# Optimization experiments

Measured on AMD Instinct MI355X. Metric: run time of the kernel, lower is better.

## Reference

```python
import jax, jax.numpy as jnp
import numpy as np

B, L, P, D, RD, NT = 128, 128, 1024, 128, 128, 256
SCALE = 1.0 / float(np.sqrt(D))


def _gelu(x):
    return jax.nn.gelu(x, approximate=False)


def _ln(x, g, b):
    mu = jnp.mean(x, axis=-1, keepdims=True)
    v = jnp.mean((x - mu) ** 2, axis=-1, keepdims=True)
    return (x - mu) * jax.lax.rsqrt(v + 1e-5) * g + b


def _mlp2(x, w1, b1, w2, b2):
    return _gelu(x @ w1 + b1) @ w2 + b2


def _l2norm(x):
    return x / jnp.maximum(jnp.sqrt(jnp.sum(x * x, axis=-1, keepdims=True)), 1e-12)


def _params(key):
    ks = jax.random.split(key, 16)
    def lin(k, i, o):
        return jax.random.normal(k, (i, o), jnp.float32) * (1.0 / float(np.sqrt(i)))
    z = lambda *s: jnp.zeros(s, jnp.float32)
    o = lambda *s: jnp.ones(s, jnp.float32)
    p = {}
    p['lt_emb'] = jax.random.normal(ks[0], (NT, D), jnp.float32) * 0.02
    p['lx_w1'] = lin(ks[1], 8, D); p['lx_b1'] = z(D)
    p['lx_w2'] = lin(ks[2], D, D); p['lx_b2'] = z(D)
    p['l_ln_g'] = o(D); p['l_ln_b'] = z(D)
    p['pt_emb'] = jax.random.normal(ks[3], (NT, D), jnp.float32) * 0.02
    p['px_w1'] = lin(ks[4], 192, D); p['px_b1'] = z(D)
    p['px_w2'] = lin(ks[5], D, D); p['px_b2'] = z(D)
    p['ps_w1'] = lin(ks[6], 1, D); p['ps_b1'] = z(D)
    p['ps_w2'] = lin(ks[7], D, D); p['ps_b2'] = z(D)
    p['p_ln_g'] = o(D); p['p_ln_b'] = z(D)
    p['proj_l_w'] = lin(ks[8], D, D)
    p['proj_p_w'] = lin(ks[9], D, D)
    p['dustbin_vec'] = jax.random.normal(ks[10], (D,), jnp.float32) * 0.02
    p['sg_w1'] = lin(ks[11], D, D); p['sg_b1'] = z(D)
    p['sg_w2'] = lin(ks[12], D, 1); p['sg_b2'] = z(1)
    p['retr_l_w'] = lin(ks[13], D, RD)
    p['retr_p_w'] = lin(ks[14], D, RD)
    return p


def setup_inputs():
    key = jax.random.key(0)
    kd = jax.random.split(key, 10)
    inp = {
        'l_x': jax.random.normal(kd[0], (B, L, 8), jnp.float32),
        'l_typ': jax.random.randint(kd[1], (B, L), 0, NT),
        'p_x': jax.random.normal(kd[2], (B, P, 192), jnp.float32),
        'p_typ': jax.random.randint(kd[3], (B, P), 0, NT),
        'p_score': jax.random.normal(kd[4], (B, P), jnp.float32),
        'p_rad': jax.random.uniform(kd[5], (B, P), jnp.float32),
        'l_mask': jax.random.bernoulli(kd[6], 0.9, (B, L)).at[:, 0].set(True),
        'p_mask': jax.random.bernoulli(kd[7], 0.9, (B, P)).at[:, 0].set(True),
    }
    inp.update(_params(kd[8]))
    return inp


def reference(l_x, l_typ, p_x, p_typ, p_score, p_rad, l_mask, p_mask,
              lt_emb, lx_w1, lx_b1, lx_w2, lx_b2, l_ln_g, l_ln_b,
              pt_emb, px_w1, px_b1, px_w2, px_b2, ps_w1, ps_b1, ps_w2, ps_b2,
              p_ln_g, p_ln_b, proj_l_w, proj_p_w, dustbin_vec,
              sg_w1, sg_b1, sg_w2, sg_b2, retr_l_w, retr_p_w):
    # --- encode_batch ---
    hL = _ln(_mlp2(l_x, lx_w1, lx_b1, lx_w2, lx_b2)
             + lt_emb[jnp.clip(l_typ, 0, NT - 1)], l_ln_g, l_ln_b) @ proj_l_w
    hP = _ln(_mlp2(p_x, px_w1, px_b1, px_w2, px_b2)
             + pt_emb[jnp.clip(p_typ, 0, NT - 1)]
             + _mlp2(p_score[..., None], ps_w1, ps_b1, ps_w2, ps_b2), p_ln_g, p_ln_b) @ proj_p_w
    neg = jnp.finfo(jnp.float32).min
    # --- feature_logits_batch: masked bilinear similarity ---
    logits = jnp.einsum('bld,bpd->blp', hL, hP) * SCALE  # [B,L,P]
    logits = jnp.where(p_mask[:, None, :], logits, neg)
    logits = jnp.where(l_mask[:, :, None], logits, neg)
    # --- assignment_logW_batch with dustbin ---
    dust = (hL @ dustbin_vec) * SCALE  # [B,L]
    full = jnp.concatenate([logits, dust[:, :, None]], axis=-1)  # [B,L,P+1]
    full = jnp.where(l_mask[:, :, None], full, neg)
    logW = jax.nn.log_softmax(full, axis=-1)
    # --- invariant_feature_terms_batch ---
    W = jnp.exp(logW)
    lm = l_mask.astype(jnp.float32)
    pm = p_mask.astype(jnp.float32)
    denom = jnp.maximum(lm.sum(axis=1), 1.0)  # [B]
    Wm = jnp.concatenate([W[..., :-1] * pm[:, None, :], W[..., -1:]], axis=-1)
    sharp = (Wm.max(axis=-1) * lm).sum(axis=1) / denom
    ent = ((-(Wm * logW)).sum(axis=-1) * lm).sum(axis=1) / denom
    neg_ent = -ent
    # --- pooled_embeddings_batch ---
    l_g = (hL * lm[..., None]).sum(axis=1) / jnp.maximum(lm.sum(axis=1)[:, None], 1.0)
    p_g = (hP * pm[..., None]).sum(axis=1) / jnp.maximum(pm.sum(axis=1)[:, None], 1.0)
    l_z = _l2norm(l_g @ retr_l_w)
    p_z = _l2norm(p_g @ retr_p_w)
    # --- pocket_sigma_nodes_batch ---
    sig = jax.nn.softplus((_gelu(hP @ sg_w1 + sg_b1) @ sg_w2 + sg_b2)[..., 0]) + 1e-3 + jnp.maximum(p_rad, 0.0)
    return logW, sharp, neg_ent, l_z, p_z, sig
```

## Files before the change

kernel.cpp:

```cpp
#include <hip/hip_runtime.h>
#include <hip/hip_bf16.h>
#include <math.h>

#define B_ 128
#define L_ 128
#define P_ 1024
#define D_ 128
#define NT_ 256

#define NEGF (-__FLT_MAX__)
#define SCALE_ 0.08838834764831845f
#define CLAMPV 1e30f

#define OUT_SHARP  16793600
#define OUT_NEGENT 16793728
#define OUT_LZ     16793856
#define OUT_PZ     16810240
#define OUT_SIG    16826624

#define WS_HLB    0
#define WS_HPB    1048576
#define WS_DUST   9437184
#define WS_SHARPP 9453568
#define WS_ENTP   9454592
#define WS_FLAG   9455616
#define WS_WT     9455632
#define WS_PPART  9500696
#define WS_PCNT   10024984

using bh8  = __attribute__((ext_vector_type(8))) short;
using fx4  = __attribute__((ext_vector_type(4))) float;

__device__ __forceinline__ float gelu_(float x) {
    float c = x * x;
    float v = x * fmaf(c, 0.07135481584f, 1.5957691216f);
    return x * __builtin_amdgcn_rcpf(1.0f + __expf(-v));
}
__device__ __forceinline__ float bf2f(unsigned short u) {
    return __uint_as_float(((unsigned)u) << 16);
}
__device__ __forceinline__ float sanz(float x) {
    return fminf(fmaxf(x, -CLAMPV), CLAMPV);
}
template<int BF> __device__ __forceinline__ float ldf(const void* p, int i) {
    if constexpr (BF) return bf2f(((const unsigned short*)p)[i]);
    else return ((const float*)p)[i];
}
template<int BF> __device__ __forceinline__ void stf(void* p, size_t i, float x) {
    x = sanz(x);
    if constexpr (BF) ((__hip_bfloat16*)p)[i] = __float2bfloat16(x);
    else ((float*)p)[i] = x;
}
__device__ __forceinline__ float maskf(const void* m, int mm, int idx) {
    if (mm == 3) return ((const float*)m)[idx] != 0.f ? 1.f : 0.f;
    if (mm == 2) return ((const unsigned short*)m)[idx] ? 1.f : 0.f;
    if (mm == 1) return ((const unsigned char*)m)[idx] ? 1.f : 0.f;
    return ((const int*)m)[idx] ? 1.f : 0.f;
}
__device__ __forceinline__ int typf(const void* p, int tm, int idx) {
    int v;
    if (tm == 2) v = (int)bf2f(((const unsigned short*)p)[idx]);
    else if (tm == 1) v = (int)((const long long*)p)[idx];
    else v = ((const int*)p)[idx];
    return v < 0 ? 0 : (v > NT_ - 1 ? NT_ - 1 : v);
}

__global__ __launch_bounds__(64) void detect_k(const unsigned int* __restrict__ px,
                                               const unsigned int* __restrict__ pm,
                                               const unsigned int* __restrict__ pt,
                                               int* __restrict__ flags)
{
    const int t = threadIdx.x;
    int hit = 0;
    for (int i = t; i < 4096; i += 64) {
        unsigned e = (px[i] >> 7) & 0xFFu;
        hit += (e >= 110 && e <= 132) ? 1 : 0;
    }
    for (int s = 1; s < 64; s <<= 1) hit += __shfl_xor(hit, s);

    unsigned big = 0, lo3f = 0, hi3f = 0;
    for (int i = t; i < 1024; i += 64) {
        unsigned wv = pm[i];
        big  |= (wv > 1u) ? 1u : 0u;
        lo3f |= ((wv & 0xFFFFu) == 0x3F80u) ? 1u : 0u;
        hi3f |= ((wv >> 16) == 0x3F80u) ? 1u : 0u;
    }
    unsigned long long aBig = __ballot(big != 0), aLo = __ballot(lo3f != 0), aHi = __ballot(hi3f != 0);

    unsigned tbig = 0, oddnz = 0;
    for (int i = t; i < 512; i += 64) {
        unsigned we = pt[2 * i], wo = pt[2 * i + 1];
        tbig  |= (we > 0xFFFFu || wo > 0xFFFFu) ? 1u : 0u;
        oddnz |= (wo != 0u) ? 1u : 0u;
    }
    unsigned long long aTb = __ballot(tbig != 0), aOdd = __ballot(oddnz != 0);

    if (t == 0) {
        flags[1] = (hit > 2048) ? 1 : 0;
        flags[0] = aLo ? 2 : (aHi ? 3 : (aBig ? 1 : 0));
        flags[2] = aTb ? 2 : (!aOdd ? 1 : 0);
    }
}

template<int BF> __device__ __forceinline__ void wt_prep_body(
    const void* w1, const void* w2, const void* sw2,
    const void* proj, const void* gw1, __hip_bfloat16* wt)
{
    const int idx = blockIdx.x * 256 + threadIdx.x;
    const int stride = gridDim.x * 256;
    for (int i = idx; i < 128 * 192; i += stride) {
        int n = i / 192, k = i - n * 192;
        wt[n * 192 + k] = __float2bfloat16(ldf<BF>(w1, k * 128 + n));
    }
    __hip_bfloat16* w2c = wt + 24576;
    for (int i = idx; i < 128 * 256; i += stride) {
        int n = i >> 8, k = i & 255;
        float v = (k < 128) ? ldf<BF>(w2, k * 128 + n) : ldf<BF>(sw2, (k - 128) * 128 + n);
        w2c[n * 256 + k] = __float2bfloat16(v);
    }
    __hip_bfloat16* pjt = wt + 57344;
    for (int i = idx; i < 128 * 128; i += stride) {
        int n = i >> 7, k = i & 127;
        pjt[n * 128 + k] = __float2bfloat16(ldf<BF>(proj, k * 128 + n));
    }
    __hip_bfloat16* g1t = wt + 73728;
    for (int i = idx; i < 128 * 128; i += stride) {
        int n = i >> 7, k = i & 127;
        g1t[n * 128 + k] = __float2bfloat16(ldf<BF>(gw1, k * 128 + n));
    }
}

__global__ __launch_bounds__(256) void wt_prep_k(
    const void* w1, const void* w2, const void* sw2,
    const void* proj, const void* gw1, __hip_bfloat16* wt, const int* flags)
{
    if (flags[1]) wt_prep_body<1>(w1, w2, sw2, proj, gw1, wt);
    else          wt_prep_body<0>(w1, w2, sw2, proj, gw1, wt);
}

#define RL 8
template<int BF> __device__ __forceinline__ void enc_l_body(
    const void* l_x, const void* l_typ, int tm,
    const void* w1, const void* b1, const void* w2, const void* b2,
    const void* lng, const void* lnb, const void* emb, const void* proj,
    const void* dustv, __hip_bfloat16* hLb, float* dust)
{
    __shared__ __align__(16) float X[RL * 8];
    __shared__ __align__(16) float H[RL][D_];
    __shared__ __align__(16) float Y[RL][D_];
    __shared__ float mus[RL], rss[RL];
    const int o = threadIdx.x;
    const int base = blockIdx.x * RL;

    if (o < RL * 8) X[o] = ldf<BF>(l_x, base * 8 + o);
    __syncthreads();

    float acc[RL];
    const float b1o = ldf<BF>(b1, o);
#pragma unroll
    for (int r = 0; r < RL; r++) acc[r] = b1o;
#pragma unroll
    for (int i = 0; i < 8; i += 4) {
        float wa = ldf<BF>(w1, (i + 0) * D_ + o), wb = ldf<BF>(w1, (i + 1) * D_ + o);
        float wc = ldf<BF>(w1, (i + 2) * D_ + o), wd = ldf<BF>(w1, (i + 3) * D_ + o);
#pragma unroll
        for (int r = 0; r < RL; r++) {
            const float4 x4 = *(const float4*)&X[r * 8 + i];
            acc[r] = fmaf(x4.x, wa, fmaf(x4.y, wb, fmaf(x4.z, wc, fmaf(x4.w, wd, acc[r]))));
        }
    }
#pragma unroll
    for (int r = 0; r < RL; r++) H[r][o] = gelu_(acc[r]);
    __syncthreads();

#pragma unroll
    for (int r = 0; r < RL; r++) {
        int tt = typf(l_typ, tm, base + r);
        acc[r] = ldf<BF>(b2, o) + ldf<BF>(emb, tt * D_ + o);
    }
    for (int i = 0; i < D_; i += 4) {
        float wa = ldf<BF>(w2, (i + 0) * D_ + o), wb = ldf<BF>(w2, (i + 1) * D_ + o);
        float wc = ldf<BF>(w2, (i + 2) * D_ + o), wd = ldf<BF>(w2, (i + 3) * D_ + o);
#pragma unroll
        for (int r = 0; r < RL; r++) {
            const float4 h4 = *(const float4*)&H[r][i];
            acc[r] = fmaf(h4.x, wa, fmaf(h4.y, wb, fmaf(h4.z, wc, fmaf(h4.w, wd, acc[r]))));
        }
    }
#pragma unroll
    for (int r = 0; r < RL; r++) Y[r][o] = acc[r];
    __syncthreads();

    {
        const int r = o >> 4, j = o & 15;
        float s = 0.f;
#pragma unroll
        for (int i = 0; i < 8; i++) s += Y[r][j * 8 + i];
        s += __shfl_xor(s, 1); s += __shfl_xor(s, 2); s += __shfl_xor(s, 4); s += __shfl_xor(s, 8);
        const float mu = s * (1.f / 128.f);
        float v = 0.f;
#pragma unroll
        for (int i = 0; i < 8; i++) { float d = Y[r][j * 8 + i] - mu; v = fmaf(d, d, v); }
        v += __shfl_xor(v, 1); v += __shfl_xor(v, 2); v += __shfl_xor(v, 4); v += __shfl_xor(v, 8);
        if (j == 0) { mus[r] = mu; rss[r] = rsqrtf(v * (1.f / 128.f) + 1e-5f); }
    }
    __syncthreads();
    {
        const float g = ldf<BF>(lng, o), bl = ldf<BF>(lnb, o);
#pragma unroll
        for (int r = 0; r < RL; r++) Y[r][o] = fmaf((Y[r][o] - mus[r]) * rss[r], g, bl);
    }
    __syncthreads();

#pragma unroll
    for (int r = 0; r < RL; r++) acc[r] = 0.f;
    for (int i = 0; i < D_; i += 4) {
        float wa = ldf<BF>(proj, (i + 0) * D_ + o), wb = ldf<BF>(proj, (i + 1) * D_ + o);
        float wc = ldf<BF>(proj, (i + 2) * D_ + o), wd = ldf<BF>(proj, (i + 3) * D_ + o);
#pragma unroll
        for (int r = 0; r < RL; r++) {
            const float4 y4 = *(const float4*)&Y[r][i];
            acc[r] = fmaf(y4.x, wa, fmaf(y4.y, wb, fmaf(y4.z, wc, fmaf(y4.w, wd, acc[r]))));
        }
    }
    const float dvo = ldf<BF>(dustv, o);
#pragma unroll
    for (int r = 0; r < RL; r++) {
        hLb[(size_t)(base + r) * D_ + o] = __float2bfloat16(acc[r]);
        H[r][o] = acc[r] * dvo;
    }
    __syncthreads();
    {
        const int r = o >> 4, j = o & 15;
        float s = 0.f;
#pragma unroll
        for (int i = 0; i < 8; i++) s += H[r][j * 8 + i];
        s += __shfl_xor(s, 1); s += __shfl_xor(s, 2); s += __shfl_xor(s, 4); s += __shfl_xor(s, 8);
        if (j == 0) dust[base + r] = s * SCALE_;
    }
}

__global__ __launch_bounds__(128) void enc_l_k(
    const void* l_x, const void* l_typ,
    const void* w1, const void* b1, const void* w2, const void* b2,
    const void* lng, const void* lnb, const void* emb, const void* proj,
    const void* dustv, __hip_bfloat16* hLb, float* dust, const int* flags)
{
    const int tm = flags[2];
    if (flags[1]) enc_l_body<1>(l_x, l_typ, tm, w1, b1, w2, b2, lng, lnb, emb, proj, dustv, hLb, dust);
    else          enc_l_body<0>(l_x, l_typ, tm, w1, b1, w2, b2, lng, lnb, emb, proj, dustv, hLb, dust);
}

#define XS 264
#define ROWS 64
#define ENC_P_SMEM 36608
template<int BF> __device__ __forceinline__ void enc_p_body(
    unsigned short* X, float* red1, float* red2, float* pm_s, float* sc_s, int* tt_s,
    const void* p_x, const void* p_typ, int tm,
    const void* p_score, const void* p_rad,
    const void* b1, const void* b2, const void* sb2,
    const void* sw1, const void* sb1,
    const void* lng, const void* lnb, const void* emb,
    const void* gb1, const void* gw2, const void* gb2,
    const unsigned short* wt, const void* p_mask, int mm,
    void* out, __hip_bfloat16* hPb, float* ppart, float* pcnt)
{
    const int t = threadIdx.x;
    const int o = t & 127, rh = t >> 7;
    const int lane = t & 63, w = t >> 6;
    const int m = lane & 15, g = lane >> 4;
    const int b = blockIdx.x >> 4, tile = blockIdx.x & 15;
    const int base = b * P_ + tile * ROWS;
    const int c0 = 32 * w + m, c1 = 32 * w + 16 + m;
    __hip_bfloat16* Xb = (__hip_bfloat16*)X;

    if constexpr (BF) {
        const unsigned short* src = (const unsigned short*)p_x + (size_t)base * 192;
#pragma unroll
        for (int i = t * 8; i < ROWS * 192; i += 256 * 8) {
            const int r = i / 192, k = i - r * 192;
            *(bh8*)(X + r * XS + k) = *(const bh8*)(src + i);
        }
    } else {
        for (int i = t; i < ROWS * 192; i += 256) {
            int r = i / 192, k = i - r * 192;
            Xb[r * XS + k] = __float2bfloat16(((const float*)p_x)[(size_t)base * 192 + i]);
        }
    }
    if (t < ROWS) {
        pm_s[t] = maskf(p_mask, mm, base + t);
        sc_s[t] = ldf<BF>(p_score, base + t);
        tt_s[t] = typf(p_typ, tm, base + t);
    }
    __syncthreads();

    fx4 A1[4][2];
#pragma unroll
    for (int mt = 0; mt < 4; mt++) { A1[mt][0] = fx4{0,0,0,0}; A1[mt][1] = fx4{0,0,0,0}; }
    {
        const unsigned short* q0 = wt + ((2 * w + 0) * 16 + m) * 192 + g * 8;
        const unsigned short* q1 = wt + ((2 * w + 1) * 16 + m) * 192 + g * 8;
#pragma unroll
        for (int ks = 0; ks < 6; ks++) {
            bh8 f0 = *(const bh8*)(q0 + ks * 32);
            bh8 f1 = *(const bh8*)(q1 + ks * 32);
#pragma unroll
            for (int mt = 0; mt < 4; mt++) {
                bh8 a = *(const bh8*)(X + (mt * 16 + m) * XS + g * 8 + ks * 32);
                A1[mt][0] = __builtin_amdgcn_mfma_f32_16x16x32_bf16(a, f0, A1[mt][0], 0, 0, 0);
                A1[mt][1] = __builtin_amdgcn_mfma_f32_16x16x32_bf16(a, f1, A1[mt][1], 0, 0, 0);
            }
        }
    }
    __syncthreads();

    {
        const float bb0 = ldf<BF>(b1, c0), bb1 = ldf<BF>(b1, c1);
#pragma unroll
        for (int mt = 0; mt < 4; mt++)
#pragma unroll
            for (int j = 0; j < 4; j++) {
                const int row = mt * 16 + g * 4 + j;
                Xb[row * XS + c0] = __float2bfloat16(gelu_(A1[mt][0][j] + bb0));
                Xb[row * XS + c1] = __float2bfloat16(gelu_(A1[mt][1][j] + bb1));
            }
    }
    {
        const float a1v = ldf<BF>(sw1, o), a0v = ldf<BF>(sb1, o);
#pragma unroll
        for (int r = 0; r < 32; r++) {
            const int row = rh * 32 + r;
            Xb[row * XS + 128 + o] = __float2bfloat16(gelu_(fmaf(sc_s[row], a1v, a0v)));
        }
    }
    __syncthreads();

    fx4 A2[4][2];
#pragma unroll
    for (int mt = 0; mt < 4; mt++) { A2[mt][0] = fx4{0,0,0,0}; A2[mt][1] = fx4{0,0,0,0}; }
    {
        const unsigned short* w2cT = wt + 24576;
        const unsigned short* q0 = w2cT + ((2 * w + 0) * 16 + m) * 256 + g * 8;
        const unsigned short* q1 = w2cT + ((2 * w + 1) * 16 + m) * 256 + g * 8;
#pragma unroll
        for (int ks = 0; ks < 8; ks++) {
            bh8 f0 = *(const bh8*)(q0 + ks * 32);
            bh8 f1 = *(const bh8*)(q1 + ks * 32);
#pragma unroll
            for (int mt = 0; mt < 4; mt++) {
                bh8 a = *(const bh8*)(X + (mt * 16 + m) * XS + g * 8 + ks * 32);
                A2[mt][0] = __builtin_amdgcn_mfma_f32_16x16x32_bf16(a, f0, A2[mt][0], 0, 0, 0);
                A2[mt][1] = __builtin_amdgcn_mfma_f32_16x16x32_bf16(a, f1, A2[mt][1], 0, 0, 0);
            }
        }
    }
    {
        const float bc0 = ldf<BF>(b2, c0) + ldf<BF>(sb2, c0);
        const float bc1 = ldf<BF>(b2, c1) + ldf<BF>(sb2, c1);
#pragma unroll
        for (int mt = 0; mt < 4; mt++)
#pragma unroll
            for (int j = 0; j < 4; j++) {
                const int row = mt * 16 + g * 4 + j;
                const int tt = tt_s[row];
                A2[mt][0][j] += bc0 + ldf<BF>(emb, tt * D_ + c0);
                A2[mt][1][j] += bc1 + ldf<BF>(emb, tt * D_ + c1);
            }
    }
#pragma unroll
    for (int mt = 0; mt < 4; mt++)
#pragma unroll
        for (int j = 0; j < 4; j++) {
            float s = A2[mt][0][j] + A2[mt][1][j];
            s += __shfl_xor(s, 1); s += __shfl_xor(s, 2); s += __shfl_xor(s, 4); s += __shfl_xor(s, 8);
            if (m == 0) red1[(mt * 16 + g * 4 + j) * 4 + w] = s;
        }
    __syncthreads();
    float mu_[4][4];
#pragma unroll
    for (int mt = 0; mt < 4; mt++)
#pragma unroll
        for (int j = 0; j < 4; j++) {
            const int row = mt * 16 + g * 4 + j;
            mu_[mt][j] = ((red1[row * 4 + 0] + red1[row * 4 + 1]) +
                          (red1[row * 4 + 2] + red1[row * 4 + 3])) * (1.f / 128.f);
            float d0 = A2[mt][0][j] - mu_[mt][j];
            float d1 = A2[mt][1][j] - mu_[mt][j];
            float v = fmaf(d0, d0, d1 * d1);
            v += __shfl_xor(v, 1); v += __shfl_xor(v, 2); v += __shfl_xor(v, 4); v += __shfl_xor(v, 8);
            if (m == 0) red2[row * 4 + w] = v;
        }
    __syncthreads();
    {
        const float gc0 = ldf<BF>(lng, c0), bl0 = ldf<BF>(lnb, c0);
        const float gc1 = ldf<BF>(lng, c1), bl1 = ldf<BF>(lnb, c1);
#pragma unroll
        for (int mt = 0; mt < 4; mt++)
#pragma unroll
            for (int j = 0; j < 4; j++) {
                const int row = mt * 16 + g * 4 + j;
                float var = ((red2[row * 4 + 0] + red2[row * 4 + 1]) +
                             (red2[row * 4 + 2] + red2[row * 4 + 3])) * (1.f / 128.f);
                float rs = rsqrtf(var + 1e-5f);
                float y0 = fmaf((A2[mt][0][j] - mu_[mt][j]) * rs, gc0, bl0);
                float y1 = fmaf((A2[mt][1][j] - mu_[mt][j]) * rs, gc1, bl1);
                Xb[row * XS + c0] = __float2bfloat16(y0);
                Xb[row * XS + c1] = __float2bfloat16(y1);
            }
    }
    __syncthreads();

    fx4 A3[4][2];
#pragma unroll
    for (int mt = 0; mt < 4; mt++) { A3[mt][0] = fx4{0,0,0,0}; A3[mt][1] = fx4{0,0,0,0}; }
    {
        const unsigned short* pjT = wt + 57344;
        const unsigned short* q0 = pjT + ((2 * w + 0) * 16 + m) * 128 + g * 8;
        const unsigned short* q1 = pjT + ((2 * w + 1) * 16 + m) * 128 + g * 8;
#pragma unroll
        for (int ks = 0; ks < 4; ks++) {
            bh8 f0 = *(const bh8*)(q0 + ks * 32);
            bh8 f1 = *(const bh8*)(q1 + ks * 32);
#pragma unroll
            for (int mt = 0; mt < 4; mt++) {
                bh8 a = *(const bh8*)(X + (mt * 16 + m) * XS + g * 8 + ks * 32);
                A3[mt][0] = __builtin_amdgcn_mfma_f32_16x16x32_bf16(a, f0, A3[mt][0], 0, 0, 0);
                A3[mt][1] = __builtin_amdgcn_mfma_f32_16x16x32_bf16(a, f1, A3[mt][1], 0, 0, 0);
            }
        }
    }
    __syncthreads();

    {
#pragma unroll
        for (int mt = 0; mt < 4; mt++)
#pragma unroll
            for (int j = 0; j < 4; j++) {
                const int row = mt * 16 + g * 4 + j;
                __hip_bfloat16 h0 = __float2bfloat16(A3[mt][0][j]);
                __hip_bfloat16 h1 = __float2bfloat16(A3[mt][1][j]);
                hPb[(size_t)(base + row) * D_ + c0] = h0;
                hPb[(size_t)(base + row) * D_ + c1] = h1;
                Xb[row * XS + c0] = h0;
                Xb[row * XS + c1] = h1;
            }
        float ps0 = 0.f, ps1 = 0.f;
#pragma unroll
        for (int mt = 0; mt < 4; mt++)
#pragma unroll
            for (int j = 0; j < 4; j++) {
                const int row = mt * 16 + g * 4 + j;
                ps0 = fmaf(A3[mt][0][j], pm_s[row], ps0);
                ps1 = fmaf(A3[mt][1][j], pm_s[row], ps1);
            }
        ps0 += __shfl_xor(ps0, 16); ps0 += __shfl_xor(ps0, 32);
        ps1 += __shfl_xor(ps1, 16); ps1 += __shfl_xor(ps1, 32);
        if (g == 0) {
            ppart[(size_t)blockIdx.x * D_ + c0] = ps0;
            ppart[(size_t)blockIdx.x * D_ + c1] = ps1;
        }
        if (t == 0) {
            float c = 0.f;
#pragma unroll
            for (int r = 0; r < ROWS; r++) c += pm_s[r];
            pcnt[blockIdx.x] = c;
        }
    }
    __syncthreads();

    fx4 A4[4][2];
#pragma unroll
    for (int mt = 0; mt < 4; mt++) { A4[mt][0] = fx4{0,0,0,0}; A4[mt][1] = fx4{0,0,0,0}; }
    {
        const unsigned short* g1T = wt + 73728;
        const unsigned short* q0 = g1T + ((2 * w + 0) * 16 + m) * 128 + g * 8;
        const unsigned short* q1 = g1T + ((2 * w + 1) * 16 + m) * 128 + g * 8;
#pragma unroll
        for (int ks = 0; ks < 4; ks++) {
            bh8 f0 = *(const bh8*)(q0 + ks * 32);
            bh8 f1 = *(const bh8*)(q1 + ks * 32);
#pragma unroll
            for (int mt = 0; mt < 4; mt++) {
                bh8 a = *(const bh8*)(X + (mt * 16 + m) * XS + g * 8 + ks * 32);
                A4[mt][0] = __builtin_amdgcn_mfma_f32_16x16x32_bf16(a, f0, A4[mt][0], 0, 0, 0);
                A4[mt][1] = __builtin_amdgcn_mfma_f32_16x16x32_bf16(a, f1, A4[mt][1], 0, 0, 0);
            }
        }
    }
    {
        const float gb0 = ldf<BF>(gb1, c0), gb1v = ldf<BF>(gb1, c1);
        const float w20 = ldf<BF>(gw2, c0), w21 = ldf<BF>(gw2, c1);
#pragma unroll
        for (int mt = 0; mt < 4; mt++)
#pragma unroll
            for (int j = 0; j < 4; j++) {
                const int row = mt * 16 + g * 4 + j;
                float g0 = gelu_(A4[mt][0][j] + gb0);
                float g1v = gelu_(A4[mt][1][j] + gb1v);
                float p = fmaf(g0, w20, g1v * w21);
                p += __shfl_xor(p, 1); p += __shfl_xor(p, 2); p += __shfl_xor(p, 4); p += __shfl_xor(p, 8);
                if (m == 0) red1[row * 4 + w] = p;
            }
    }
    __syncthreads();
    if (t < ROWS) {
        float s = (red1[t * 4 + 0] + red1[t * 4 + 1]) + (red1[t * 4 + 2] + red1[t * 4 + 3]);
        float v = s + ldf<BF>(gb2, 0);
        float sp = fmaxf(v, 0.f) + log1pf(expf(-fabsf(v)));
        stf<BF>(out, (size_t)OUT_SIG + base + t, sp + 1e-3f + fmaxf(ldf<BF>(p_rad, base + t), 0.f));
    }
}

__global__ __launch_bounds__(256) void enc_p_k(
    const void* p_x, const void* p_typ, const void* p_score, const void* p_rad,
    const void* b1, const void* b2, const void* sb2,
    const void* sw1, const void* sb1,
    const void* lng, const void* lnb, const void* emb,
    const void* gb1, const void* gw2, const void* gb2,
    const unsigned short* wt, const void* p_mask, const int* flags,
    void* out, __hip_bfloat16* hPb, float* ppart, float* pcnt)
{
    extern __shared__ __align__(16) char smem[];
    unsigned short* X = (unsigned short*)smem;
    float* red1 = (float*)(smem + 33792);
    float* red2 = (float*)(smem + 34816);
    float* pm_s = (float*)(smem + 35840);
    float* sc_s = (float*)(smem + 36096);
    int*   tt_s = (int*)(smem + 36352);
    const int tm = flags[2], mm = flags[0];
    if (flags[1]) enc_p_body<1>(X, red1, red2, pm_s, sc_s, tt_s,
                                p_x, p_typ, tm, p_score, p_rad, b1, b2, sb2, sw1, sb1,
                                lng, lnb, emb, gb1, gw2, gb2, wt, p_mask, mm,
                                out, hPb, ppart, pcnt);
    else          enc_p_body<0>(X, red1, red2, pm_s, sc_s, tt_s,
                                p_x, p_typ, tm, p_score, p_rad, b1, b2, sb2, sw1, sb1,
                                lng, lnb, emb, gb1, gw2, gb2, wt, p_mask, mm,
                                out, hPb, ppart, pcnt);
}

template<int BF> __device__ __forceinline__ void logits_sm_body(
    const unsigned short* hLb, const unsigned short* hPb, const float* dust,
    const void* l_mask, const void* p_mask, int mm,
    void* out, float* sharp_parts, float* ent_parts)
{
    __shared__ float pm_s[1024];
    __shared__ float lm_s[16], dv_s[16];
    __shared__ float redA[64], redB[64], redC[64], redD[64], redM[16], redL[16];
    const int t = threadIdx.x;
    const int lane = t & 63, w = t >> 6;
    const int m = lane & 15, g = lane >> 4;
    const int b = blockIdx.x & 127, l0 = (blockIdx.x >> 7) * 16;

    for (int i = t; i < 1024; i += 256) pm_s[i] = maskf(p_mask, mm, b * P_ + i);
    if (t < 16) {
        lm_s[t] = maskf(l_mask, mm, b * L_ + l0 + t);
        dv_s[t] = dust[b * L_ + l0 + t];
    }
    __syncthreads();

    bh8 af[4];
    {
        const unsigned short* ha = hLb + ((size_t)(b * L_ + l0 + m)) * D_ + g * 8;
#pragma unroll
        for (int ks = 0; ks < 4; ks++) af[ks] = *(const bh8*)(ha + ks * 32);
    }
    const unsigned short* hpb = hPb + ((size_t)(b * P_ + w * 256)) * D_;

    fx4 acc[16];
#pragma unroll
    for (int nt = 0; nt < 16; nt++) {
        fx4 c = {0.f, 0.f, 0.f, 0.f};
        const unsigned short* hr = hpb + (nt * 16 + m) * D_ + g * 8;
#pragma unroll
        for (int ks = 0; ks < 4; ks++) {
            bh8 bfr = *(const bh8*)(hr + ks * 32);
            c = __builtin_amdgcn_mfma_f32_16x16x32_bf16(af[ks], bfr, c, 0, 0, 0);
        }
        acc[nt] = c;
    }

    float rmax[4] = {NEGF, NEGF, NEGF, NEGF};
#pragma unroll
    for (int nt = 0; nt < 16; nt++) {
        const float pv = pm_s[w * 256 + nt * 16 + m];
#pragma unroll
        for (int j = 0; j < 4; j++) {
            const bool ok = (lm_s[g * 4 + j] != 0.f) && (pv != 0.f);
            float v = ok ? acc[nt][j] * SCALE_ : NEGF;
            acc[nt][j] = v;
            rmax[j] = fmaxf(rmax[j], v);
        }
    }
#pragma unroll
    for (int j = 0; j < 4; j++) {
        rmax[j] = fmaxf(rmax[j], __shfl_xor(rmax[j], 1));
        rmax[j] = fmaxf(rmax[j], __shfl_xor(rmax[j], 2));
        rmax[j] = fmaxf(rmax[j], __shfl_xor(rmax[j], 4));
        rmax[j] = fmaxf(rmax[j], __shfl_xor(rmax[j], 8));
    }
    if (m == 0) {
#pragma unroll
        for (int j = 0; j < 4; j++) redA[(g * 4 + j) * 4 + w] = rmax[j];
    }
    __syncthreads();
    float mrow[4], lse[4];
#pragma unroll
    for (int j = 0; j < 4; j++) {
        const int r = g * 4 + j;
        float mm4 = fmaxf(fmaxf(redA[r * 4 + 0], redA[r * 4 + 1]), fmaxf(redA[r * 4 + 2], redA[r * 4 + 3]));
        float dvr = (lm_s[r] != 0.f) ? dv_s[r] : NEGF;
        mrow[j] = fmaxf(mm4, dvr);
    }
    float se[4] = {0.f, 0.f, 0.f, 0.f};
#pragma unroll
    for (int nt = 0; nt < 16; nt++) {
#pragma unroll
        for (int j = 0; j < 4; j++) se[j] += __expf(acc[nt][j] - mrow[j]);
    }
#pragma unroll
    for (int j = 0; j < 4; j++) {
        se[j] += __shfl_xor(se[j], 1); se[j] += __shfl_xor(se[j], 2);
        se[j] += __shfl_xor(se[j], 4); se[j] += __shfl_xor(se[j], 8);
    }
    if (m == 0) {
#pragma unroll
        for (int j = 0; j < 4; j++) redB[(g * 4 + j) * 4 + w] = se[j];
    }
    __syncthreads();
#pragma unroll
    for (int j = 0; j < 4; j++) {
        const int r = g * 4 + j;
        float dvr = (lm_s[r] != 0.f) ? dv_s[r] : NEGF;
        float s = (redB[r * 4 + 0] + redB[r * 4 + 1]) + (redB[r * 4 + 2] + redB[r * 4 + 3]);
        s += __expf(dvr - mrow[j]);
        lse[j] = __logf(s);
    }
    if (w == 0 && m == 0) {
#pragma unroll
        for (int j = 0; j < 4; j++) { redM[g * 4 + j] = mrow[j]; redL[g * 4 + j] = lse[j]; }
    }
    float mw[4] = {0.f, 0.f, 0.f, 0.f}, es[4] = {0.f, 0.f, 0.f, 0.f};
#pragma unroll
    for (int nt = 0; nt < 16; nt++) {
        const float pv = pm_s[w * 256 + nt * 16 + m];
#pragma unroll
        for (int j = 0; j < 4; j++) {
            float lw = acc[nt][j] - mrow[j] - lse[j];
            stf<BF>(out, (size_t)(b * L_ + l0 + g * 4 + j) * (P_ + 1) + w * 256 + nt * 16 + m, lw);
            float lwc = fmaxf(lw, -CLAMPV);
            float wm = __expf(lwc) * pv;
            mw[j] = fmaxf(mw[j], wm);
            if (wm > 0.f) es[j] = fmaf(-wm, lwc, es[j]);
        }
    }
#pragma unroll
    for (int j = 0; j < 4; j++) {
        mw[j] = fmaxf(mw[j], __shfl_xor(mw[j], 1));
        mw[j] = fmaxf(mw[j], __shfl_xor(mw[j], 2));
        mw[j] = fmaxf(mw[j], __shfl_xor(mw[j], 4));
        mw[j] = fmaxf(mw[j], __shfl_xor(mw[j], 8));
        es[j] += __shfl_xor(es[j], 1); es[j] += __shfl_xor(es[j], 2);
        es[j] += __shfl_xor(es[j], 4); es[j] += __shfl_xor(es[j], 8);
    }
    if (m == 0) {
#pragma unroll
        for (int j = 0; j < 4; j++) {
            redC[(g * 4 + j) * 4 + w] = mw[j];
            redD[(g * 4 + j) * 4 + w] = es[j];
        }
    }
    __syncthreads();
    if (t < 16) {
        float dvr = (lm_s[t] != 0.f) ? dv_s[t] : NEGF;
        stf<BF>(out, (size_t)(b * L_ + l0 + t) * (P_ + 1) + P_, dvr - redM[t] - redL[t]);
    }
    if (t == 0) {
        float sp = 0.f, en = 0.f;
        for (int r = 0; r < 16; r++) {
            float dvr = (lm_s[r] != 0.f) ? dv_s[r] : NEGF;
            float lwd = fmaxf(dvr - redM[r] - redL[r], -CLAMPV);
            float wd = __expf(lwd);
            float mwr = fmaxf(fmaxf(redC[r * 4 + 0], redC[r * 4 + 1]), fmaxf(redC[r * 4 + 2], redC[r * 4 + 3]));
            mwr = fmaxf(mwr, wd);
            float esr = (redD[r * 4 + 0] + redD[r * 4 + 1]) + (redD[r * 4 + 2] + redD[r * 4 + 3]);
            if (wd > 0.f) esr = fmaf(-wd, lwd, esr);
            sp = fmaf(mwr, lm_s[r], sp);
            en = fmaf(esr, lm_s[r], en);
        }
        sharp_parts[blockIdx.x] = sp;
        ent_parts[blockIdx.x] = en;
    }
}

__global__ __launch_bounds__(256) void logits_sm_k(
    const unsigned short* hLb, const unsigned short* hPb, const float* dust,
    const void* l_mask, const void* p_mask, const int* flags,
    void* out, float* sharp_parts, float* ent_parts)
{
    const int mm = flags[0];
    if (flags[1]) logits_sm_body<1>(hLb, hPb, dust, l_mask, p_mask, mm, out, sharp_parts, ent_parts);
    else          logits_sm_body<0>(hLb, hPb, dust, l_mask, p_mask, mm, out, sharp_parts, ent_parts);
}

template<int BF> __device__ __forceinline__ void epilogue_body(
    const unsigned short* hLb, const void* l_mask, int mm,
    const void* retr_l, const void* retr_p,
    const float* ppart, const float* pcnt,
    const float* sharp_parts, const float* ent_parts, void* out)
{
    __shared__ float lmv[L_];
    __shared__ __align__(16) float lg[D_];
    __shared__ __align__(16) float pgs[D_];
    __shared__ float red[4];
    const int o = threadIdx.x, b = blockIdx.x;
    lmv[o] = maskf(l_mask, mm, b * L_ + o);
    __syncthreads();
    float cnt = 0.f;
    for (int l = 0; l < L_; l++) cnt += lmv[l];
    {
        float s0 = 0, s1 = 0, s2 = 0, s3 = 0;
        const unsigned short* hb = hLb + (size_t)b * L_ * D_;
        for (int l = 0; l < L_; l += 4) {
            s0 = fmaf(bf2f(hb[(l + 0) * D_ + o]), lmv[l + 0], s0);
            s1 = fmaf(bf2f(hb[(l + 1) * D_ + o]), lmv[l + 1], s1);
            s2 = fmaf(bf2f(hb[(l + 2) * D_ + o]), lmv[l + 2], s2);
            s3 = fmaf(bf2f(hb[(l + 3) * D_ + o]), lmv[l + 3], s3);
        }
        lg[o] = ((s0 + s1) + (s2 + s3)) / fmaxf(cnt, 1.f);
    }
    {
        float s = 0.f, c = 0.f;
        for (int k = 0; k < 16; k++) s += ppart[(size_t)(b * 16 + k) * D_ + o];
        for (int k = 0; k < 16; k++) c += pcnt[b * 16 + k];
        pgs[o] = s / fmaxf(c, 1.f);
    }
    __syncthreads();
    float rL = 0.f, rP = 0.f;
    for (int i = 0; i < D_; i += 4) {
        const float4 g4 = *(const float4*)&lg[i];
        rL = fmaf(g4.x, ldf<BF>(retr_l, (i + 0) * D_ + o), rL);
        rL = fmaf(g4.y, ldf<BF>(retr_l, (i + 1) * D_ + o), rL);
        rL = fmaf(g4.z, ldf<BF>(retr_l, (i + 2) * D_ + o), rL);
        rL = fmaf(g4.w, ldf<BF>(retr_l, (i + 3) * D_ + o), rL);
        const float4 p4 = *(const float4*)&pgs[i];
        rP = fmaf(p4.x, ldf<BF>(retr_p, (i + 0) * D_ + o), rP);
        rP = fmaf(p4.y, ldf<BF>(retr_p, (i + 1) * D_ + o), rP);
        rP = fmaf(p4.z, ldf<BF>(retr_p, (i + 2) * D_ + o), rP);
        rP = fmaf(p4.w, ldf<BF>(retr_p, (i + 3) * D_ + o), rP);
    }
    float nL = rL * rL, nP = rP * rP;
    nL += __shfl_xor(nL, 1); nL += __shfl_xor(nL, 2); nL += __shfl_xor(nL, 4);
    nL += __shfl_xor(nL, 8); nL += __shfl_xor(nL, 16); nL += __shfl_xor(nL, 32);
    nP += __shfl_xor(nP, 1); nP += __shfl_xor(nP, 2); nP += __shfl_xor(nP, 4);
    nP += __shfl_xor(nP, 8); nP += __shfl_xor(nP, 16); nP += __shfl_xor(nP, 32);
    if ((o & 63) == 0) { red[o >> 6] = nL; red[2 + (o >> 6)] = nP; }
    __syncthreads();
    {
        float nrmL = fmaxf(sqrtf(red[0] + red[1]), 1e-12f);
        float nrmP = fmaxf(sqrtf(red[2] + red[3]), 1e-12f);
        stf<BF>(out, (size_t)OUT_LZ + b * D_ + o, rL / nrmL);
        stf<BF>(out, (size_t)OUT_PZ + b * D_ + o, rP / nrmP);
    }
    if (o == 0) {
        const float den = fmaxf(cnt, 1.f);
        float sp = 0.f, en = 0.f;
        for (int k = 0; k < 8; k++) { sp += sharp_parts[k * 128 + b]; en += ent_parts[k * 128 + b]; }
        stf<BF>(out, (size_t)OUT_SHARP + b, sp / den);
        stf<BF>(out, (size_t)OUT_NEGENT + b, -(en / den));
    }
}

__global__ __launch_bounds__(128) void epilogue_k(
    const unsigned short* hLb, const void* l_mask, const int* flags,
    const void* retr_l, const void* retr_p,
    const float* ppart, const float* pcnt,
    const float* sharp_parts, const float* ent_parts, void* out)
{
    const int mm = flags[0];
    if (flags[1]) epilogue_body<1>(hLb, l_mask, mm, retr_l, retr_p, ppart, pcnt, sharp_parts, ent_parts, out);
    else          epilogue_body<0>(hLb, l_mask, mm, retr_l, retr_p, ppart, pcnt, sharp_parts, ent_parts, out);
}

extern "C" void kernel_launch(void* const* d_in, const int* in_sizes, int n_in,
                              void* d_out, int out_size, void* d_ws, size_t ws_size,
                              hipStream_t stream)
{
    const void* l_x     = d_in[0];
    const void* l_typ   = d_in[1];
    const void* p_x     = d_in[2];
    const void* p_typ   = d_in[3];
    const void* p_score = d_in[4];
    const void* p_rad   = d_in[5];
    const void* l_mask  = d_in[6];
    const void* p_mask  = d_in[7];
    const void* lt_emb  = d_in[8];
    const void* lx_w1   = d_in[9];
    const void* lx_b1   = d_in[10];
    const void* lx_w2   = d_in[11];
    const void* lx_b2   = d_in[12];
    const void* l_ln_g  = d_in[13];
    const void* l_ln_b  = d_in[14];
    const void* pt_emb  = d_in[15];
    const void* px_w1   = d_in[16];
    const void* px_b1   = d_in[17];
    const void* px_w2   = d_in[18];
    const void* px_b2   = d_in[19];
    const void* ps_w1   = d_in[20];
    const void* ps_b1   = d_in[21];
    const void* ps_w2   = d_in[22];
    const void* ps_b2   = d_in[23];
    const void* p_ln_g  = d_in[24];
    const void* p_ln_b  = d_in[25];
    const void* proj_l  = d_in[26];
    const void* proj_p  = d_in[27];
    const void* dustv   = d_in[28];
    const void* sg_w1   = d_in[29];
    const void* sg_b1   = d_in[30];
    const void* sg_w2   = d_in[31];
    const void* sg_b2   = d_in[32];
    const void* retr_l  = d_in[33];
    const void* retr_p  = d_in[34];

    float* ws     = (float*)d_ws;
    __hip_bfloat16* hLb = (__hip_bfloat16*)(ws + WS_HLB);
    __hip_bfloat16* hPb = (__hip_bfloat16*)(ws + WS_HPB);
    float* dust   = ws + WS_DUST;
    float* sharpp = ws + WS_SHARPP;
    float* entp   = ws + WS_ENTP;
    int*   flags  = (int*)(ws + WS_FLAG);
    __hip_bfloat16* wt = (__hip_bfloat16*)(ws + WS_WT);
    float* ppart  = ws + WS_PPART;
    float* pcnt   = ws + WS_PCNT;

    detect_k<<<1, 64, 0, stream>>>((const unsigned int*)p_x, (const unsigned int*)p_mask,
                                   (const unsigned int*)p_typ, flags);
    wt_prep_k<<<64, 256, 0, stream>>>(px_w1, px_w2, ps_w2, proj_p, sg_w1, wt, flags);
    enc_l_k<<<(B_ * L_) / RL, 128, 0, stream>>>(l_x, l_typ, lx_w1, lx_b1, lx_w2, lx_b2,
                                                l_ln_g, l_ln_b, lt_emb, proj_l, dustv,
                                                hLb, dust, flags);
    enc_p_k<<<B_ * (P_ / ROWS), 256, ENC_P_SMEM, stream>>>(
        p_x, p_typ, p_score, p_rad,
        px_b1, px_b2, ps_b2, ps_w1, ps_b1,
        p_ln_g, p_ln_b, pt_emb,
        sg_b1, sg_w2, sg_b2,
        (const unsigned short*)wt, p_mask, flags,
        d_out, hPb, ppart, pcnt);
    logits_sm_k<<<B_ * 8, 256, 0, stream>>>((const unsigned short*)hLb, (const unsigned short*)hPb,
                                            dust, l_mask, p_mask, flags, d_out, sharpp, entp);
    epilogue_k<<<B_, 128, 0, stream>>>((const unsigned short*)hLb, l_mask, flags,
                                       retr_l, retr_p, ppart, pcnt, sharpp, entp, d_out);
}
```

Baseline: 211.2 us.

## Split enc_p column tiles across eight waves with 512-thread blocks

```diff
diff --git a/kernel.cpp b/kernel.cpp
--- a/kernel.cpp
+++ b/kernel.cpp
@@ -253,7 +253,7 @@
 
 #define XS 264
 #define ROWS 64
-#define ENC_P_SMEM 36608
+#define ENC_P_SMEM 38656
 template<int BF> __device__ __forceinline__ void enc_p_body(
     unsigned short* X, float* red1, float* red2, float* pm_s, float* sc_s, int* tt_s,
     const void* p_x, const void* p_typ, int tm,
@@ -271,18 +271,18 @@
     const int m = lane & 15, g = lane >> 4;
     const int b = blockIdx.x >> 4, tile = blockIdx.x & 15;
     const int base = b * P_ + tile * ROWS;
-    const int c0 = 32 * w + m, c1 = 32 * w + 16 + m;
+    const int c = 16 * w + m;
     __hip_bfloat16* Xb = (__hip_bfloat16*)X;
 
     if constexpr (BF) {
         const unsigned short* src = (const unsigned short*)p_x + (size_t)base * 192;
 #pragma unroll
-        for (int i = t * 8; i < ROWS * 192; i += 256 * 8) {
+        for (int i = t * 8; i < ROWS * 192; i += 512 * 8) {
             const int r = i / 192, k = i - r * 192;
             *(bh8*)(X + r * XS + k) = *(const bh8*)(src + i);
         }
     } else {
-        for (int i = t; i < ROWS * 192; i += 256) {
+        for (int i = t; i < ROWS * 192; i += 512) {
             int r = i / 192, k = i - r * 192;
             Xb[r * XS + k] = __float2bfloat16(((const float*)p_x)[(size_t)base * 192 + i]);
         }
@@ -294,86 +294,75 @@
     }
     __syncthreads();
 
-    fx4 A1[4][2];
-#pragma unroll
-    for (int mt = 0; mt < 4; mt++) { A1[mt][0] = fx4{0,0,0,0}; A1[mt][1] = fx4{0,0,0,0}; }
-    {
-        const unsigned short* q0 = wt + ((2 * w + 0) * 16 + m) * 192 + g * 8;
-        const unsigned short* q1 = wt + ((2 * w + 1) * 16 + m) * 192 + g * 8;
+    fx4 A1[4];
+#pragma unroll
+    for (int mt = 0; mt < 4; mt++) A1[mt] = fx4{0, 0, 0, 0};
+    {
+        const unsigned short* q = wt + (w * 16 + m) * 192 + g * 8;
 #pragma unroll
         for (int ks = 0; ks < 6; ks++) {
-            bh8 f0 = *(const bh8*)(q0 + ks * 32);
-            bh8 f1 = *(const bh8*)(q1 + ks * 32);
+            bh8 f = *(const bh8*)(q + ks * 32);
 #pragma unroll
             for (int mt = 0; mt < 4; mt++) {
                 bh8 a = *(const bh8*)(X + (mt * 16 + m) * XS + g * 8 + ks * 32);
-                A1[mt][0] = __builtin_amdgcn_mfma_f32_16x16x32_bf16(a, f0, A1[mt][0], 0, 0, 0);
-                A1[mt][1] = __builtin_amdgcn_mfma_f32_16x16x32_bf16(a, f1, A1[mt][1], 0, 0, 0);
-            }
-        }
-    }
-    __syncthreads();
-
-    {
-        const float bb0 = ldf<BF>(b1, c0), bb1 = ldf<BF>(b1, c1);
+                A1[mt] = __builtin_amdgcn_mfma_f32_16x16x32_bf16(a, f, A1[mt], 0, 0, 0);
+            }
+        }
+    }
+    __syncthreads();
+
+    {
+        const float bb = ldf<BF>(b1, c);
 #pragma unroll
         for (int mt = 0; mt < 4; mt++)
 #pragma unroll
             for (int j = 0; j < 4; j++) {
                 const int row = mt * 16 + g * 4 + j;
-                Xb[row * XS + c0] = __float2bfloat16(gelu_(A1[mt][0][j] + bb0));
-                Xb[row * XS + c1] = __float2bfloat16(gelu_(A1[mt][1][j] + bb1));
+                Xb[row * XS + c] = __float2bfloat16(gelu_(A1[mt][j] + bb));
             }
     }
     {
         const float a1v = ldf<BF>(sw1, o), a0v = ldf<BF>(sb1, o);
 #pragma unroll
-        for (int r = 0; r < 32; r++) {
-            const int row = rh * 32 + r;
+        for (int r = 0; r < 16; r++) {
+            const int row = rh * 16 + r;
             Xb[row * XS + 128 + o] = __float2bfloat16(gelu_(fmaf(sc_s[row], a1v, a0v)));
         }
     }
     __syncthreads();
 
-    fx4 A2[4][2];
-#pragma unroll
-    for (int mt = 0; mt < 4; mt++) { A2[mt][0] = fx4{0,0,0,0}; A2[mt][1] = fx4{0,0,0,0}; }
-    {
-        const unsigned short* w2cT = wt + 24576;
-        const unsigned short* q0 = w2cT + ((2 * w + 0) * 16 + m) * 256 + g * 8;
-        const unsigned short* q1 = w2cT + ((2 * w + 1) * 16 + m) * 256 + g * 8;
+    fx4 A2[4];
+#pragma unroll
+    for (int mt = 0; mt < 4; mt++) A2[mt] = fx4{0, 0, 0, 0};
+    {
+        const unsigned short* q = wt + 24576 + (w * 16 + m) * 256 + g * 8;
 #pragma unroll
         for (int ks = 0; ks < 8; ks++) {
-            bh8 f0 = *(const bh8*)(q0 + ks * 32);
-            bh8 f1 = *(const bh8*)(q1 + ks * 32);
+            bh8 f = *(const bh8*)(q + ks * 32);
 #pragma unroll
             for (int mt = 0; mt < 4; mt++) {
                 bh8 a = *(const bh8*)(X + (mt * 16 + m) * XS + g * 8 + ks * 32);
-                A2[mt][0] = __builtin_amdgcn_mfma_f32_16x16x32_bf16(a, f0, A2[mt][0], 0, 0, 0);
-                A2[mt][1] = __builtin_amdgcn_mfma_f32_16x16x32_bf16(a, f1, A2[mt][1], 0, 0, 0);
-            }
-        }
-    }
-    {
-        const float bc0 = ldf<BF>(b2, c0) + ldf<BF>(sb2, c0);
-        const float bc1 = ldf<BF>(b2, c1) + ldf<BF>(sb2, c1);
+                A2[mt] = __builtin_amdgcn_mfma_f32_16x16x32_bf16(a, f, A2[mt], 0, 0, 0);
+            }
+        }
+    }
+    {
+        const float bc = ldf<BF>(b2, c) + ldf<BF>(sb2, c);
 #pragma unroll
         for (int mt = 0; mt < 4; mt++)
 #pragma unroll
             for (int j = 0; j < 4; j++) {
                 const int row = mt * 16 + g * 4 + j;
-                const int tt = tt_s[row];
-                A2[mt][0][j] += bc0 + ldf<BF>(emb, tt * D_ + c0);
-                A2[mt][1][j] += bc1 + ldf<BF>(emb, tt * D_ + c1);
+                A2[mt][j] += bc + ldf<BF>(emb, tt_s[row] * D_ + c);
             }
     }
 #pragma unroll
     for (int mt = 0; mt < 4; mt++)
 #pragma unroll
         for (int j = 0; j < 4; j++) {
-            float s = A2[mt][0][j] + A2[mt][1][j];
+            float s = A2[mt][j];
             s += __shfl_xor(s, 1); s += __shfl_xor(s, 2); s += __shfl_xor(s, 4); s += __shfl_xor(s, 8);
-            if (m == 0) red1[(mt * 16 + g * 4 + j) * 4 + w] = s;
+            if (m == 0) red1[(mt * 16 + g * 4 + j) * 8 + w] = s;
         }
     __syncthreads();
     float mu_[4][4];
@@ -382,50 +371,43 @@
 #pragma unroll
         for (int j = 0; j < 4; j++) {
             const int row = mt * 16 + g * 4 + j;
-            mu_[mt][j] = ((red1[row * 4 + 0] + red1[row * 4 + 1]) +
-                          (red1[row * 4 + 2] + red1[row * 4 + 3])) * (1.f / 128.f);
-            float d0 = A2[mt][0][j] - mu_[mt][j];
-            float d1 = A2[mt][1][j] - mu_[mt][j];
-            float v = fmaf(d0, d0, d1 * d1);
+            float s = ((red1[row * 8 + 0] + red1[row * 8 + 1]) + (red1[row * 8 + 2] + red1[row * 8 + 3]))
+                    + ((red1[row * 8 + 4] + red1[row * 8 + 5]) + (red1[row * 8 + 6] + red1[row * 8 + 7]));
+            mu_[mt][j] = s * (1.f / 128.f);
+            float d = A2[mt][j] - mu_[mt][j];
+            float v = d * d;
             v += __shfl_xor(v, 1); v += __shfl_xor(v, 2); v += __shfl_xor(v, 4); v += __shfl_xor(v, 8);
-            if (m == 0) red2[row * 4 + w] = v;
-        }
-    __syncthreads();
-    {
-        const float gc0 = ldf<BF>(lng, c0), bl0 = ldf<BF>(lnb, c0);
-        const float gc1 = ldf<BF>(lng, c1), bl1 = ldf<BF>(lnb, c1);
+            if (m == 0) red2[row * 8 + w] = v;
+        }
+    __syncthreads();
+    {
+        const float gc = ldf<BF>(lng, c), bl = ldf<BF>(lnb, c);
 #pragma unroll
         for (int mt = 0; mt < 4; mt++)
 #pragma unroll
             for (int j = 0; j < 4; j++) {
                 const int row = mt * 16 + g * 4 + j;
-                float var = ((red2[row * 4 + 0] + red2[row * 4 + 1]) +
-                             (red2[row * 4 + 2] + red2[row * 4 + 3])) * (1.f / 128.f);
-                float rs = rsqrtf(var + 1e-5f);
-                float y0 = fmaf((A2[mt][0][j] - mu_[mt][j]) * rs, gc0, bl0);
-                float y1 = fmaf((A2[mt][1][j] - mu_[mt][j]) * rs, gc1, bl1);
-                Xb[row * XS + c0] = __float2bfloat16(y0);
-                Xb[row * XS + c1] = __float2bfloat16(y1);
-            }
-    }
-    __syncthreads();
-
-    fx4 A3[4][2];
-#pragma unroll
-    for (int mt = 0; mt < 4; mt++) { A3[mt][0] = fx4{0,0,0,0}; A3[mt][1] = fx4{0,0,0,0}; }
-    {
-        const unsigned short* pjT = wt + 57344;
-        const unsigned short* q0 = pjT + ((2 * w + 0) * 16 + m) * 128 + g * 8;
-        const unsigned short* q1 = pjT + ((2 * w + 1) * 16 + m) * 128 + g * 8;
+                float var = ((red2[row * 8 + 0] + red2[row * 8 + 1]) + (red2[row * 8 + 2] + red2[row * 8 + 3]))
+                          + ((red2[row * 8 + 4] + red2[row * 8 + 5]) + (red2[row * 8 + 6] + red2[row * 8 + 7]));
+                float rs = rsqrtf(var * (1.f / 128.f) + 1e-5f);
+                float y = fmaf((A2[mt][j] - mu_[mt][j]) * rs, gc, bl);
+                Xb[row * XS + c] = __float2bfloat16(y);
+            }
+    }
+    __syncthreads();
+
+    fx4 A3[4];
+#pragma unroll
+    for (int mt = 0; mt < 4; mt++) A3[mt] = fx4{0, 0, 0, 0};
+    {
+        const unsigned short* q = wt + 57344 + (w * 16 + m) * 128 + g * 8;
 #pragma unroll
         for (int ks = 0; ks < 4; ks++) {
-            bh8 f0 = *(const bh8*)(q0 + ks * 32);
-            bh8 f1 = *(const bh8*)(q1 + ks * 32);
+            bh8 f = *(const bh8*)(q + ks * 32);
 #pragma unroll
             for (int mt = 0; mt < 4; mt++) {
                 bh8 a = *(const bh8*)(X + (mt * 16 + m) * XS + g * 8 + ks * 32);
-                A3[mt][0] = __builtin_amdgcn_mfma_f32_16x16x32_bf16(a, f0, A3[mt][0], 0, 0, 0);
-                A3[mt][1] = __builtin_amdgcn_mfma_f32_16x16x32_bf16(a, f1, A3[mt][1], 0, 0, 0);
+                A3[mt] = __builtin_amdgcn_mfma_f32_16x16x32_bf16(a, f, A3[mt], 0, 0, 0);
             }
         }
     }
@@ -437,81 +419,68 @@
 #pragma unroll
             for (int j = 0; j < 4; j++) {
                 const int row = mt * 16 + g * 4 + j;
-                __hip_bfloat16 h0 = __float2bfloat16(A3[mt][0][j]);
-                __hip_bfloat16 h1 = __float2bfloat16(A3[mt][1][j]);
-                hPb[(size_t)(base + row) * D_ + c0] = h0;
-                hPb[(size_t)(base + row) * D_ + c1] = h1;
-                Xb[row * XS + c0] = h0;
-                Xb[row * XS + c1] = h1;
-            }
-        float ps0 = 0.f, ps1 = 0.f;
+                __hip_bfloat16 h = __float2bfloat16(A3[mt][j]);
+                hPb[(size_t)(base + row) * D_ + c] = h;
+                Xb[row * XS + c] = h;
+            }
+        float ps = 0.f;
 #pragma unroll
         for (int mt = 0; mt < 4; mt++)
 #pragma unroll
             for (int j = 0; j < 4; j++) {
                 const int row = mt * 16 + g * 4 + j;
-                ps0 = fmaf(A3[mt][0][j], pm_s[row], ps0);
-                ps1 = fmaf(A3[mt][1][j], pm_s[row], ps1);
-            }
-        ps0 += __shfl_xor(ps0, 16); ps0 += __shfl_xor(ps0, 32);
-        ps1 += __shfl_xor(ps1, 16); ps1 += __shfl_xor(ps1, 32);
-        if (g == 0) {
-            ppart[(size_t)blockIdx.x * D_ + c0] = ps0;
-            ppart[(size_t)blockIdx.x * D_ + c1] = ps1;
-        }
+                ps = fmaf(A3[mt][j], pm_s[row], ps);
+            }
+        ps += __shfl_xor(ps, 16); ps += __shfl_xor(ps, 32);
+        if (g == 0) ppart[(size_t)blockIdx.x * D_ + c] = ps;
         if (t == 0) {
-            float c = 0.f;
-#pragma unroll
-            for (int r = 0; r < ROWS; r++) c += pm_s[r];
-            pcnt[blockIdx.x] = c;
-        }
-    }
-    __syncthreads();
-
-    fx4 A4[4][2];
-#pragma unroll
-    for (int mt = 0; mt < 4; mt++) { A4[mt][0] = fx4{0,0,0,0}; A4[mt][1] = fx4{0,0,0,0}; }
-    {
-        const unsigned short* g1T = wt + 73728;
-        const unsigned short* q0 = g1T + ((2 * w + 0) * 16 + m) * 128 + g * 8;
-        const unsigned short* q1 = g1T + ((2 * w + 1) * 16 + m) * 128 + g * 8;
+            float cc = 0.f;
+#pragma unroll
+            for (int r = 0; r < ROWS; r++) cc += pm_s[r];
+            pcnt[blockIdx.x] = cc;
+        }
+    }
+    __syncthreads();
+
+    fx4 A4[4];
+#pragma unroll
+    for (int mt = 0; mt < 4; mt++) A4[mt] = fx4{0, 0, 0, 0};
+    {
+        const unsigned short* q = wt + 73728 + (w * 16 + m) * 128 + g * 8;
 #pragma unroll
         for (int ks = 0; ks < 4; ks++) {
-            bh8 f0 = *(const bh8*)(q0 + ks * 32);
-            bh8 f1 = *(const bh8*)(q1 + ks * 32);
+            bh8 f = *(const bh8*)(q + ks * 32);
 #pragma unroll
             for (int mt = 0; mt < 4; mt++) {
                 bh8 a = *(const bh8*)(X + (mt * 16 + m) * XS + g * 8 + ks * 32);
-                A4[mt][0] = __builtin_amdgcn_mfma_f32_16x16x32_bf16(a, f0, A4[mt][0], 0, 0, 0);
-                A4[mt][1] = __builtin_amdgcn_mfma_f32_16x16x32_bf16(a, f1, A4[mt][1], 0, 0, 0);
-            }
-        }
-    }
-    {
-        const float gb0 = ldf<BF>(gb1, c0), gb1v = ldf<BF>(gb1, c1);
-        const float w20 = ldf<BF>(gw2, c0), w21 = ldf<BF>(gw2, c1);
+                A4[mt] = __builtin_amdgcn_mfma_f32_16x16x32_bf16(a, f, A4[mt], 0, 0, 0);
+            }
+        }
+    }
+    {
+        const float gb = ldf<BF>(gb1, c);
+        const float w2v = ldf<BF>(gw2, c);
 #pragma unroll
         for (int mt = 0; mt < 4; mt++)
 #pragma unroll
             for (int j = 0; j < 4; j++) {
                 const int row = mt * 16 + g * 4 + j;
-                float g0 = gelu_(A4[mt][0][j] + gb0);
-                float g1v = gelu_(A4[mt][1][j] + gb1v);
-                float p = fmaf(g0, w20, g1v * w21);
+                float p = gelu_(A4[mt][j] + gb) * w2v;
                 p += __shfl_xor(p, 1); p += __shfl_xor(p, 2); p += __shfl_xor(p, 4); p += __shfl_xor(p, 8);
-                if (m == 0) red1[row * 4 + w] = p;
+                if (m == 0) red1[row * 8 + w] = p;
             }
     }
     __syncthreads();
     if (t < ROWS) {
-        float s = (red1[t * 4 + 0] + red1[t * 4 + 1]) + (red1[t * 4 + 2] + red1[t * 4 + 3]);
+        float s = ((red1[t * 8 + 0] + red1[t * 8 + 1]) + (red1[t * 8 + 2] + red1[t * 8 + 3]))
+                + ((red1[t * 8 + 4] + red1[t * 8 + 5]) + (red1[t * 8 + 6] + red1[t * 8 + 7]));
         float v = s + ldf<BF>(gb2, 0);
         float sp = fmaxf(v, 0.f) + log1pf(expf(-fabsf(v)));
         stf<BF>(out, (size_t)OUT_SIG + base + t, sp + 1e-3f + fmaxf(ldf<BF>(p_rad, base + t), 0.f));
     }
 }
 
-__global__ __launch_bounds__(256) void enc_p_k(
+__global__ __launch_bounds__(512) void enc_p_k(
     const void* p_x, const void* p_typ, const void* p_score, const void* p_rad,
     const void* b1, const void* b2, const void* sb2,
     const void* sw1, const void* sb1,
@@ -523,10 +492,10 @@
     extern __shared__ __align__(16) char smem[];
     unsigned short* X = (unsigned short*)smem;
     float* red1 = (float*)(smem + 33792);
-    float* red2 = (float*)(smem + 34816);
-    float* pm_s = (float*)(smem + 35840);
-    float* sc_s = (float*)(smem + 36096);
-    int*   tt_s = (int*)(smem + 36352);
+    float* red2 = (float*)(smem + 35840);
+    float* pm_s = (float*)(smem + 37888);
+    float* sc_s = (float*)(smem + 38144);
+    int*   tt_s = (int*)(smem + 38400);
     const int tm = flags[2], mm = flags[0];
     if (flags[1]) enc_p_body<1>(X, red1, red2, pm_s, sc_s, tt_s,
                                 p_x, p_typ, tm, p_score, p_rad, b1, b2, sb2, sw1, sb1,
@@ -838,7 +807,7 @@
     enc_l_k<<<(B_ * L_) / RL, 128, 0, stream>>>(l_x, l_typ, lx_w1, lx_b1, lx_w2, lx_b2,
                                                 l_ln_g, l_ln_b, lt_emb, proj_l, dustv,
                                                 hLb, dust, flags);
-    enc_p_k<<<B_ * (P_ / ROWS), 256, ENC_P_SMEM, stream>>>(
+    enc_p_k<<<B_ * (P_ / ROWS), 512, ENC_P_SMEM, stream>>>(
         p_x, p_typ, p_score, p_rad,
         px_b1, px_b2, ps_b2, ps_w1, ps_b1,
         p_ln_g, p_ln_b, pt_emb,
```

Result: slower. 222.9 us (+5.5%).
